# Kernel tuning notes

Hardware: AMD Instinct MI355X
Metric: run time of the kernel (lower is better)

Reference implementation:

```python
import jax, jax.numpy as jnp
import numpy as np

B, T, D, F, E, K = 2, 2048, 1024, 4096, 8, 2

def setup_inputs() -> dict:
    key = jax.random.key(0)
    k0, k1, k2, k3 = jax.random.split(key, 4)
    return {
        "x": jax.random.normal(k0, (B, T, D), jnp.float32),
        "Wg": jax.random.normal(k1, (D, E), jnp.float32) * (D ** -0.5),
        "W1": jax.random.normal(k2, (E, D, F), jnp.float32) * (D ** -0.5),
        "b1": jnp.zeros((E, F), jnp.float32),
        "W2": jax.random.normal(k3, (E, F, D), jnp.float32) * (F ** -0.5),
        "b2": jnp.zeros((E, D), jnp.float32),
        "topk": K,
    }

def reference(x, Wg, W1, b1, W2, b2, topk):
    n_experts = Wg.shape[-1]
    # Gating logits [B, T, E]
    gating = jnp.einsum('btd,de->bte', x, Wg)
    _, idx = jax.lax.top_k(gating, topk)
    # 0/1 mask of selected experts per token [B, T, E]
    mask = jax.nn.one_hot(idx, n_experts, dtype=x.dtype).sum(axis=-2)
    # Source does `gating -= 1/mask - 1`: no-op where mask==1, -inf where mask==0
    gate = jax.nn.softmax(jnp.where(mask > 0, gating, -jnp.inf), axis=-1)
    # Dense masked per-expert compute, exactly as the source (expert(x * mask_e))
    xm = x[:, :, None, :] * mask[:, :, :, None]          # [B, T, E, D]
    h = jax.nn.gelu(jnp.einsum('bted,edf->btef', xm, W1) + b1)  # [B, T, E, F]
    out_e = jnp.einsum('btef,efd->bted', h, W2) + b2     # [B, T, E, D]
    # Gate and sum over experts
    return jnp.sum(out_e * gate[..., None], axis=-2)      # [B, T, D]
```

## Files before the change

kernel.cpp:

```cpp
#include <hip/hip_runtime.h>
#include <hip/hip_bf16.h>
#include <math.h>

#define NB 2
#define NT 2048
#define NTOK 4096
#define DD 1024
#define FF 4096
#define NE 8
#define KSEL 2
#define BM 128
#define BN 128
#define BK 64
#define ROWCAP 9216
#define ROWTILES 72
#define KP2 2

typedef __attribute__((ext_vector_type(8))) short short8_t;
typedef __attribute__((ext_vector_type(4))) float f32x4;

__device__ __forceinline__ unsigned short f2bf(float f){
  unsigned u = __float_as_uint(f);
  unsigned r = (u + 0x7fffu + ((u >> 16) & 1u)) >> 16;
  return (unsigned short)r;
}

__device__ __forceinline__ int xcd_swz(int lin, int nwg){
  int q = nwg >> 3, r = nwg & 7;
  int xcd = lin & 7, idx = lin >> 3;
  return (xcd < r ? xcd * (q + 1) : r * (q + 1) + (xcd - r) * q) + idx;
}

#define GLOAD_LDS(g, l) \
  __builtin_amdgcn_global_load_lds((const __attribute__((address_space(1))) void*)(g), \
                                   (__attribute__((address_space(3))) void*)(l), 16, 0, 0)


__global__ void k_prep(const float* __restrict__ x, const float* __restrict__ wg,
                       short* __restrict__ xb, int* __restrict__ topk_idx,
                       float* __restrict__ topk_gate, int* __restrict__ counts){
  int wid = threadIdx.x >> 6, lane = threadIdx.x & 63;
  int t = blockIdx.x * 4 + wid;
  const float* xr = x + (size_t)t * DD;
  short* xbr = xb + (size_t)t * DD;
  double acc[NE];
#pragma unroll
  for (int e = 0; e < NE; ++e) acc[e] = 0.0;
#pragma unroll
  for (int p = 0; p < 4; ++p){
    int d = p * 256 + lane * 4;
    float4 v = *(const float4*)(xr + d);
    short4 o;
    o.x = (short)f2bf(v.x); o.y = (short)f2bf(v.y);
    o.z = (short)f2bf(v.z); o.w = (short)f2bf(v.w);
    *(short4*)(xbr + d) = o;
    const float* w0 = wg + (size_t)d * NE;
    float vv[4] = {v.x, v.y, v.z, v.w};
#pragma unroll
    for (int j = 0; j < 4; ++j){
      double xv = (double)vv[j];
#pragma unroll
      for (int e = 0; e < NE; ++e) acc[e] += xv * (double)w0[j * NE + e];
    }
  }
#pragma unroll
  for (int e = 0; e < NE; ++e){
#pragma unroll
    for (int s = 32; s; s >>= 1) acc[e] += __shfl_xor(acc[e], s, 64);
  }
  if (lane == 0){
    int i0 = 0; double v0 = acc[0];
#pragma unroll
    for (int e = 1; e < NE; ++e) if (acc[e] > v0){ v0 = acc[e]; i0 = e; }
    int i1 = -1; double v1 = -1e300;
#pragma unroll
    for (int e = 0; e < NE; ++e) if (e != i0 && acc[e] > v1){ v1 = acc[e]; i1 = e; }
    double g0 = 1.0 / (1.0 + exp(v1 - v0));
    topk_idx[2 * t] = i0; topk_idx[2 * t + 1] = i1;
    topk_gate[2 * t] = (float)g0; topk_gate[2 * t + 1] = (float)(1.0 - g0);
    atomicAdd(&counts[i0], 1);
    atomicAdd(&counts[i1], 1);
  }
}


__global__ void k_transpose_all(const float* __restrict__ W1, const float* __restrict__ W2,
                                short* __restrict__ w1t, short* __restrict__ w2t){
  __shared__ short T[64][132];
  int id = blockIdx.x;
  bool isW2 = id >= 4096;
  int rem = id & 4095;
  int e = rem >> 9;
  int tr = rem & 511;
  int R, C, c0, r0;
  const float* in; short* out;
  if (!isW2){ R = DD; C = FF; c0 = (tr & 63) * 64; r0 = (tr >> 6) * 128;
              in = W1 + (size_t)e * R * C; out = w1t + (size_t)e * R * C; }
  else      { R = FF; C = DD; c0 = (tr & 15) * 64; r0 = (tr >> 4) * 128;
              in = W2 + (size_t)e * R * C; out = w2t + (size_t)e * R * C; }
  int t = threadIdx.x;
  int rr = t >> 4, c4 = (t & 15) * 4;
#pragma unroll
  for (int p = 0; p < 8; ++p){
    int row = p * 16 + rr;
    float4 v = *(const float4*)(in + (size_t)(r0 + row) * C + c0 + c4);
    T[c4 + 0][row] = (short)f2bf(v.x);
    T[c4 + 1][row] = (short)f2bf(v.y);
    T[c4 + 2][row] = (short)f2bf(v.z);
    T[c4 + 3][row] = (short)f2bf(v.w);
  }
  __syncthreads();
  int c8 = (t & 15) * 8;
#pragma unroll
  for (int q = 0; q < 4; ++q){
    int orow = q * 16 + rr;
    short4 lo = *(const short4*)&T[orow][c8];
    short4 hi = *(const short4*)&T[orow][c8 + 4];
    short8_t w;
    w[0] = lo.x; w[1] = lo.y; w[2] = lo.z; w[3] = lo.w;
    w[4] = hi.x; w[5] = hi.y; w[6] = hi.z; w[7] = hi.w;
    *(short8_t*)(out + (size_t)(c0 + orow) * R + r0 + c8) = w;
  }
}


__global__ void k_route_all(const int* __restrict__ counts, const int* __restrict__ topk_idx,
                            const float* __restrict__ topk_gate, int* __restrict__ poff_g,
                            int* __restrict__ row_token, float* __restrict__ row_gate,
                            int* __restrict__ slot_of){
  __shared__ int poff[NE + 1], cur[NE], rends[NE];
  if (threadIdx.x == 0){
    int off = 0;
    for (int e = 0; e < NE; ++e){
      poff[e] = off; cur[e] = off; rends[e] = off + counts[e];
      off += (counts[e] + BM - 1) & ~(BM - 1);
    }
    poff[NE] = off;
    for (int e = 0; e <= NE; ++e) poff_g[e] = poff[e];
  }
  __syncthreads();
  for (int t = threadIdx.x; t < NTOK; t += 256){
#pragma unroll
    for (int k = 0; k < KSEL; ++k){
      int e = topk_idx[2 * t + k];
      float g = topk_gate[2 * t + k];
      int slot = atomicAdd(&cur[e], 1);
      row_token[slot] = t;
      row_gate[slot] = g;
      slot_of[2 * t + k] = slot;
    }
  }
  __syncthreads();
#pragma unroll
  for (int e = 0; e < NE; ++e)
    for (int s = rends[e] + (int)threadIdx.x; s < poff[e + 1]; s += 256){
      row_token[s] = 0; row_gate[s] = 0.f;
    }
}


__launch_bounds__(256, 4)
__global__ void k_gemm1(const short* __restrict__ xb, const short* __restrict__ w1t,
                        const float* __restrict__ b1, short* __restrict__ h,
                        const int* __restrict__ row_token, const int* __restrict__ poff){
  __shared__ short As[BM * BK];
  __shared__ short Bs[BN * BK];
  int wg = xcd_swz(blockIdx.x, ROWTILES * (FF / BN));
  int g = wg >> 6, t6 = wg & 63;
  int bx = (g >> 2) * 8 + (t6 & 7);
  int by = (g & 3) * 8 + (t6 >> 3);
  int row0 = bx * BM;
  if (row0 >= poff[NE]) return;
  int e = 0;
  while (row0 >= poff[e + 1]) ++e;
  int n0 = by * BN;
  int tid = threadIdx.x;

  const short* asrc[4]; const short* bsrc[4];
#pragma unroll
  for (int p = 0; p < 4; ++p){
    int L = p * 256 + tid;
    int r = L >> 3, cs = L & 7;
    int cd = cs ^ (r & 7);
    int tok = row_token[row0 + r];
    asrc[p] = xb + (size_t)tok * DD + cd * 8;
    bsrc[p] = w1t + (size_t)e * FF * DD + (size_t)(n0 + r) * DD + cd * 8;
  }
  short* alds = As + tid * 8;
  short* blds = Bs + tid * 8;

  f32x4 acc[4][4];
#pragma unroll
  for (int i = 0; i < 4; ++i)
#pragma unroll
    for (int j = 0; j < 4; ++j) acc[i][j] = (f32x4){0.f, 0.f, 0.f, 0.f};

  int wid = tid >> 6, lane = tid & 63;
  int wr = wid >> 1, wc = wid & 1;
  int lrow = lane & 15, lk = lane >> 4;

  for (int k0 = 0; k0 < DD; k0 += BK){
#pragma unroll
    for (int p = 0; p < 4; ++p){
      GLOAD_LDS(asrc[p] + k0, alds + p * 2048);
      GLOAD_LDS(bsrc[p] + k0, blds + p * 2048);
    }
    __syncthreads();
#pragma unroll
    for (int kk = 0; kk < 2; ++kk){
      short8_t a[4], b[4];
      int c = kk * 4 + lk;
#pragma unroll
      for (int m = 0; m < 4; ++m){
        int r = wr * 64 + m * 16 + lrow;
        a[m] = *(const short8_t*)(As + r * BK + ((c ^ (r & 7)) * 8));
      }
#pragma unroll
      for (int n = 0; n < 4; ++n){
        int r = wc * 64 + n * 16 + lrow;
        b[n] = *(const short8_t*)(Bs + r * BK + ((c ^ (r & 7)) * 8));
      }
#pragma unroll
      for (int m = 0; m < 4; ++m)
#pragma unroll
        for (int n = 0; n < 4; ++n)
          acc[m][n] = __builtin_amdgcn_mfma_f32_16x16x32_bf16(a[m], b[n], acc[m][n], 0, 0, 0);
    }
    __syncthreads();
  }

  const float* b1e = b1 + (size_t)e * FF;
  float bias[4];
#pragma unroll
  for (int n = 0; n < 4; ++n) bias[n] = b1e[n0 + wc * 64 + n * 16 + lrow];
#pragma unroll
  for (int m = 0; m < 4; ++m){
#pragma unroll
    for (int j = 0; j < 4; ++j){
      int row = row0 + wr * 64 + m * 16 + lk * 4 + j;
      short* hr = h + (size_t)row * FF + n0 + wc * 64 + lrow;
#pragma unroll
      for (int n = 0; n < 4; ++n){
        float v = acc[m][n][j] + bias[n];
        float u = 0.7978845608028654f * (v + 0.044715f * v * v * v);
        float gl = v / (1.0f + __expf(-2.0f * u));
        hr[n * 16] = (short)f2bf(gl);
      }
    }
  }
}


__launch_bounds__(256, 4)
__global__ void k_gemm2(const short* __restrict__ h, const short* __restrict__ w2t,
                        const float* __restrict__ b2, float* __restrict__ ya,
                        float* __restrict__ yb, const int* __restrict__ poff){
  __shared__ short As[BM * BK];
  __shared__ short Bs[BN * BK];
  int wg = xcd_swz(blockIdx.x, ROWTILES * (DD / BN) * KP2);
  int kz = wg / (ROWTILES * (DD / BN));
  int c5 = wg % (ROWTILES * (DD / BN));
  int g = c5 >> 5, t5 = c5 & 31;
  int bx = g * 4 + (t5 & 3);
  int by = t5 >> 2;
  int row0 = bx * BM;
  if (row0 >= poff[NE]) return;
  int e = 0;
  while (row0 >= poff[e + 1]) ++e;
  int n0 = by * BN;
  int tid = threadIdx.x;

  const short* asrc[4]; const short* bsrc[4];
#pragma unroll
  for (int p = 0; p < 4; ++p){
    int L = p * 256 + tid;
    int r = L >> 3, cs = L & 7;
    int cd = cs ^ (r & 7);
    asrc[p] = h + (size_t)(row0 + r) * FF + cd * 8;
    bsrc[p] = w2t + (size_t)e * DD * FF + (size_t)(n0 + r) * FF + cd * 8;
  }
  short* alds = As + tid * 8;
  short* blds = Bs + tid * 8;

  f32x4 acc[4][4];
#pragma unroll
  for (int i = 0; i < 4; ++i)
#pragma unroll
    for (int j = 0; j < 4; ++j) acc[i][j] = (f32x4){0.f, 0.f, 0.f, 0.f};

  int wid = tid >> 6, lane = tid & 63;
  int wr = wid >> 1, wc = wid & 1;
  int lrow = lane & 15, lk = lane >> 4;

  int kbeg = kz * (FF / KP2), kend = kbeg + FF / KP2;
  for (int k0 = kbeg; k0 < kend; k0 += BK){
#pragma unroll
    for (int p = 0; p < 4; ++p){
      GLOAD_LDS(asrc[p] + k0, alds + p * 2048);
      GLOAD_LDS(bsrc[p] + k0, blds + p * 2048);
    }
    __syncthreads();
#pragma unroll
    for (int kk = 0; kk < 2; ++kk){
      short8_t a[4], b[4];
      int c = kk * 4 + lk;
#pragma unroll
      for (int m = 0; m < 4; ++m){
        int r = wr * 64 + m * 16 + lrow;
        a[m] = *(const short8_t*)(As + r * BK + ((c ^ (r & 7)) * 8));
      }
#pragma unroll
      for (int n = 0; n < 4; ++n){
        int r = wc * 64 + n * 16 + lrow;
        b[n] = *(const short8_t*)(Bs + r * BK + ((c ^ (r & 7)) * 8));
      }
#pragma unroll
      for (int m = 0; m < 4; ++m)
#pragma unroll
        for (int n = 0; n < 4; ++n)
          acc[m][n] = __builtin_amdgcn_mfma_f32_16x16x32_bf16(a[m], b[n], acc[m][n], 0, 0, 0);
    }
    __syncthreads();
  }

  float* y = (kz == 0) ? ya : yb;
  const float* b2e = b2 + (size_t)e * DD;
  float bias[4];
#pragma unroll
  for (int n = 0; n < 4; ++n) bias[n] = (kz == 0) ? b2e[n0 + wc * 64 + n * 16 + lrow] : 0.0f;
#pragma unroll
  for (int m = 0; m < 4; ++m){
#pragma unroll
    for (int j = 0; j < 4; ++j){
      int row = row0 + wr * 64 + m * 16 + lk * 4 + j;
      float* yr = y + (size_t)row * DD + n0 + wc * 64 + lrow;
#pragma unroll
      for (int n = 0; n < 4; ++n)
        yr[n * 16] = acc[m][n][j] + bias[n];
    }
  }
}


__global__ void k_combine(const float* __restrict__ ya, const float* __restrict__ yb,
                          const int* __restrict__ slot_of, const float* __restrict__ topk_gate,
                          float* __restrict__ out){
  int i = blockIdx.x * 256 + threadIdx.x;
  int t = i >> 8;
  int c4 = (i & 255) * 4;
  int s0 = slot_of[2 * t], s1 = slot_of[2 * t + 1];
  float g0 = topk_gate[2 * t], g1 = topk_gate[2 * t + 1];
  float4 a0 = *(const float4*)(ya + (size_t)s0 * DD + c4);
  float4 b0 = *(const float4*)(yb + (size_t)s0 * DD + c4);
  float4 a1 = *(const float4*)(ya + (size_t)s1 * DD + c4);
  float4 b1 = *(const float4*)(yb + (size_t)s1 * DD + c4);
  float4 o;
  o.x = g0 * (a0.x + b0.x) + g1 * (a1.x + b1.x);
  o.y = g0 * (a0.y + b0.y) + g1 * (a1.y + b1.y);
  o.z = g0 * (a0.z + b0.z) + g1 * (a1.z + b1.z);
  o.w = g0 * (a0.w + b0.w) + g1 * (a1.w + b1.w);
  *(float4*)(out + (size_t)t * DD + c4) = o;
}


extern "C" void kernel_launch(void* const* d_in, const int* in_sizes, int n_in,
                              void* d_out, int out_size, void* d_ws, size_t ws_size,
                              hipStream_t stream){
  (void)in_sizes; (void)n_in; (void)out_size; (void)ws_size;
  const float* x  = (const float*)d_in[0];
  const float* Wg = (const float*)d_in[1];
  const float* W1 = (const float*)d_in[2];
  const float* b1 = (const float*)d_in[3];
  const float* W2 = (const float*)d_in[4];
  const float* b2 = (const float*)d_in[5];
  float* out = (float*)d_out;
  char* ws = (char*)d_ws;

  int*   counts    = (int*)(ws + 0);
  int*   poff      = (int*)(ws + 256);
  int*   topk_idx  = (int*)(ws + 1024);
  float* topk_gate = (float*)(ws + 33792);
  int*   row_token = (int*)(ws + 66560);
  float* row_gate  = (float*)(ws + 103424);
  int*   slot_of   = (int*)(ws + 140288);
  short* xb        = (short*)(ws + 173056);
  short* w1t       = (short*)(ws + 8561664);
  short* w2t       = (short*)(ws + 75670528);
  short* h         = (short*)(ws + 142779392);
  float* ya        = (float*)(ws + 173056);
  float* yb        = (float*)(ws + 37921792);

  hipMemsetAsync(counts, 0, 32, stream);

  k_prep<<<dim3(NTOK / 4), 256, 0, stream>>>(x, Wg, xb, topk_idx, topk_gate, counts);
  k_transpose_all<<<dim3(8192), 256, 0, stream>>>(W1, W2, w1t, w2t);
  k_route_all<<<dim3(1), 256, 0, stream>>>(counts, topk_idx, topk_gate, poff,
                                           row_token, row_gate, slot_of);
  k_gemm1<<<dim3(ROWTILES * (FF / BN)), 256, 0, stream>>>(xb, w1t, b1, h, row_token, poff);
  k_gemm2<<<dim3(ROWTILES * (DD / BN) * KP2), 256, 0, stream>>>(h, w2t, b2, ya, yb, poff);
  k_combine<<<dim3(NTOK * DD / 4 / 256), 256, 0, stream>>>(ya, yb, slot_of, topk_gate, out);
}
```

Before: 470.1 us.

## Double-buffer LDS tiles in both expert GEMMs with BK halved

Measured after the change: 437.9 us. 1.07x faster.

```diff
diff --git a/kernel.cpp b/kernel.cpp
--- a/kernel.cpp
+++ b/kernel.cpp
@@ -11,7 +11,7 @@
 #define KSEL 2
 #define BM 128
 #define BN 128
-#define BK 64
+#define BK 32
 #define ROWCAP 9216
 #define ROWTILES 72
 #define KP2 2
@@ -34,6 +34,8 @@
 #define GLOAD_LDS(g, l) \
   __builtin_amdgcn_global_load_lds((const __attribute__((address_space(1))) void*)(g), \
                                    (__attribute__((address_space(3))) void*)(l), 16, 0, 0)
+#define VMCNT0 asm volatile("s_waitcnt vmcnt(0)" ::: "memory")
+#define RAWBAR __builtin_amdgcn_s_barrier()
 
 
 __global__ void k_prep(const float* __restrict__ x, const float* __restrict__ wg,
@@ -163,8 +165,8 @@
 __global__ void k_gemm1(const short* __restrict__ xb, const short* __restrict__ w1t,
                         const float* __restrict__ b1, short* __restrict__ h,
                         const int* __restrict__ row_token, const int* __restrict__ poff){
-  __shared__ short As[BM * BK];
-  __shared__ short Bs[BN * BK];
+  __shared__ short As[2][BM * BK];
+  __shared__ short Bs[2][BN * BK];
   int wg = xcd_swz(blockIdx.x, ROWTILES * (FF / BN));
   int g = wg >> 6, t6 = wg & 63;
   int bx = (g >> 2) * 8 + (t6 & 7);
@@ -176,18 +178,16 @@
   int n0 = by * BN;
   int tid = threadIdx.x;
 
-  const short* asrc[4]; const short* bsrc[4];
-#pragma unroll
-  for (int p = 0; p < 4; ++p){
+  const short* asrc[2]; const short* bsrc[2];
+#pragma unroll
+  for (int p = 0; p < 2; ++p){
     int L = p * 256 + tid;
-    int r = L >> 3, cs = L & 7;
-    int cd = cs ^ (r & 7);
+    int r = L >> 2, c = L & 3;
+    int cd = c ^ (r & 3);
     int tok = row_token[row0 + r];
     asrc[p] = xb + (size_t)tok * DD + cd * 8;
     bsrc[p] = w1t + (size_t)e * FF * DD + (size_t)(n0 + r) * DD + cd * 8;
   }
-  short* alds = As + tid * 8;
-  short* blds = Bs + tid * 8;
 
   f32x4 acc[4][4];
 #pragma unroll
@@ -199,34 +199,41 @@
   int wr = wid >> 1, wc = wid & 1;
   int lrow = lane & 15, lk = lane >> 4;
 
-  for (int k0 = 0; k0 < DD; k0 += BK){
-#pragma unroll
-    for (int p = 0; p < 4; ++p){
-      GLOAD_LDS(asrc[p] + k0, alds + p * 2048);
-      GLOAD_LDS(bsrc[p] + k0, blds + p * 2048);
-    }
-    __syncthreads();
-#pragma unroll
-    for (int kk = 0; kk < 2; ++kk){
-      short8_t a[4], b[4];
-      int c = kk * 4 + lk;
-#pragma unroll
-      for (int m = 0; m < 4; ++m){
-        int r = wr * 64 + m * 16 + lrow;
-        a[m] = *(const short8_t*)(As + r * BK + ((c ^ (r & 7)) * 8));
-      }
-#pragma unroll
-      for (int n = 0; n < 4; ++n){
-        int r = wc * 64 + n * 16 + lrow;
-        b[n] = *(const short8_t*)(Bs + r * BK + ((c ^ (r & 7)) * 8));
-      }
-#pragma unroll
-      for (int m = 0; m < 4; ++m)
-#pragma unroll
-        for (int n = 0; n < 4; ++n)
-          acc[m][n] = __builtin_amdgcn_mfma_f32_16x16x32_bf16(a[m], b[n], acc[m][n], 0, 0, 0);
-    }
-    __syncthreads();
+  auto STAGE = [&](int nb, int k0){
+#pragma unroll
+    for (int p = 0; p < 2; ++p){
+      GLOAD_LDS(asrc[p] + k0, &As[nb][0] + tid * 8 + p * 2048);
+      GLOAD_LDS(bsrc[p] + k0, &Bs[nb][0] + tid * 8 + p * 2048);
+    }
+  };
+
+  STAGE(0, 0);
+  VMCNT0; RAWBAR;
+
+  const int NKT = DD / BK;
+#pragma unroll 1
+  for (int kt = 0; kt < NKT; ++kt){
+    int b = kt & 1;
+    bool more = (kt + 1 < NKT);
+    if (more) STAGE(b ^ 1, (kt + 1) * BK);
+    short8_t a[4], bb[4];
+#pragma unroll
+    for (int m = 0; m < 4; ++m){
+      int r = wr * 64 + m * 16 + lrow;
+      a[m] = *(const short8_t*)(&As[b][0] + r * BK + ((lk ^ (r & 3)) * 8));
+    }
+#pragma unroll
+    for (int n = 0; n < 4; ++n){
+      int r = wc * 64 + n * 16 + lrow;
+      bb[n] = *(const short8_t*)(&Bs[b][0] + r * BK + ((lk ^ (r & 3)) * 8));
+    }
+#pragma unroll
+    for (int m = 0; m < 4; ++m)
+#pragma unroll
+      for (int n = 0; n < 4; ++n)
+        acc[m][n] = __builtin_amdgcn_mfma_f32_16x16x32_bf16(a[m], bb[n], acc[m][n], 0, 0, 0);
+    if (more) VMCNT0;
+    RAWBAR;
   }
 
   const float* b1e = b1 + (size_t)e * FF;
@@ -255,8 +262,8 @@
 __global__ void k_gemm2(const short* __restrict__ h, const short* __restrict__ w2t,
                         const float* __restrict__ b2, float* __restrict__ ya,
                         float* __restrict__ yb, const int* __restrict__ poff){
-  __shared__ short As[BM * BK];
-  __shared__ short Bs[BN * BK];
+  __shared__ short As[2][BM * BK];
+  __shared__ short Bs[2][BN * BK];
   int wg = xcd_swz(blockIdx.x, ROWTILES * (DD / BN) * KP2);
   int kz = wg / (ROWTILES * (DD / BN));
   int c5 = wg % (ROWTILES * (DD / BN));
@@ -270,17 +277,15 @@
   int n0 = by * BN;
   int tid = threadIdx.x;
 
-  const short* asrc[4]; const short* bsrc[4];
-#pragma unroll
-  for (int p = 0; p < 4; ++p){
+  const short* asrc[2]; const short* bsrc[2];
+#pragma unroll
+  for (int p = 0; p < 2; ++p){
     int L = p * 256 + tid;
-    int r = L >> 3, cs = L & 7;
-    int cd = cs ^ (r & 7);
+    int r = L >> 2, c = L & 3;
+    int cd = c ^ (r & 3);
     asrc[p] = h + (size_t)(row0 + r) * FF + cd * 8;
     bsrc[p] = w2t + (size_t)e * DD * FF + (size_t)(n0 + r) * FF + cd * 8;
   }
-  short* alds = As + tid * 8;
-  short* blds = Bs + tid * 8;
 
   f32x4 acc[4][4];
 #pragma unroll
@@ -292,35 +297,42 @@
   int wr = wid >> 1, wc = wid & 1;
   int lrow = lane & 15, lk = lane >> 4;
 
-  int kbeg = kz * (FF / KP2), kend = kbeg + FF / KP2;
-  for (int k0 = kbeg; k0 < kend; k0 += BK){
-#pragma unroll
-    for (int p = 0; p < 4; ++p){
-      GLOAD_LDS(asrc[p] + k0, alds + p * 2048);
-      GLOAD_LDS(bsrc[p] + k0, blds + p * 2048);
-    }
-    __syncthreads();
-#pragma unroll
-    for (int kk = 0; kk < 2; ++kk){
-      short8_t a[4], b[4];
-      int c = kk * 4 + lk;
-#pragma unroll
-      for (int m = 0; m < 4; ++m){
-        int r = wr * 64 + m * 16 + lrow;
-        a[m] = *(const short8_t*)(As + r * BK + ((c ^ (r & 7)) * 8));
-      }
-#pragma unroll
-      for (int n = 0; n < 4; ++n){
-        int r = wc * 64 + n * 16 + lrow;
-        b[n] = *(const short8_t*)(Bs + r * BK + ((c ^ (r & 7)) * 8));
-      }
-#pragma unroll
-      for (int m = 0; m < 4; ++m)
-#pragma unroll
-        for (int n = 0; n < 4; ++n)
-          acc[m][n] = __builtin_amdgcn_mfma_f32_16x16x32_bf16(a[m], b[n], acc[m][n], 0, 0, 0);
-    }
-    __syncthreads();
+  auto STAGE = [&](int nb, int k0){
+#pragma unroll
+    for (int p = 0; p < 2; ++p){
+      GLOAD_LDS(asrc[p] + k0, &As[nb][0] + tid * 8 + p * 2048);
+      GLOAD_LDS(bsrc[p] + k0, &Bs[nb][0] + tid * 8 + p * 2048);
+    }
+  };
+
+  int kbeg = kz * (FF / KP2);
+  STAGE(0, kbeg);
+  VMCNT0; RAWBAR;
+
+  const int NKT = (FF / KP2) / BK;
+#pragma unroll 1
+  for (int kt = 0; kt < NKT; ++kt){
+    int b = kt & 1;
+    bool more = (kt + 1 < NKT);
+    if (more) STAGE(b ^ 1, kbeg + (kt + 1) * BK);
+    short8_t a[4], bb[4];
+#pragma unroll
+    for (int m = 0; m < 4; ++m){
+      int r = wr * 64 + m * 16 + lrow;
+      a[m] = *(const short8_t*)(&As[b][0] + r * BK + ((lk ^ (r & 3)) * 8));
+    }
+#pragma unroll
+    for (int n = 0; n < 4; ++n){
+      int r = wc * 64 + n * 16 + lrow;
+      bb[n] = *(const short8_t*)(&Bs[b][0] + r * BK + ((lk ^ (r & 3)) * 8));
+    }
+#pragma unroll
+    for (int m = 0; m < 4; ++m)
+#pragma unroll
+      for (int n = 0; n < 4; ++n)
+        acc[m][n] = __builtin_amdgcn_mfma_f32_16x16x32_bf16(a[m], bb[n], acc[m][n], 0, 0, 0);
+    if (more) VMCNT0;
+    RAWBAR;
   }
 
   float* y = (kz == 0) ? ya : yb;
```
